# Kernel optimization log

Hardware: AMD Instinct MI355X
Metric: run time of the kernel (lower is better)

Reference implementation:

```python
import jax, jax.numpy as jnp
import numpy as np

B, S, H = 4, 128, 768
OUT, TAG = 24, 4


def setup_inputs() -> dict:
    key = jax.random.key(0)
    k1, k2, k3, k4, k5 = jax.random.split(key, 5)
    x = jax.random.normal(k1, (B, S, H), dtype=jnp.float32)
    # linear1: in 2H -> out 3H ; linear2: in 3H -> out TAG*OUT
    s1 = 1.0 / np.sqrt(2 * H)
    s2 = 1.0 / np.sqrt(3 * H)
    W1 = jax.random.uniform(k2, (2 * H, 3 * H), minval=-s1, maxval=s1, dtype=jnp.float32)
    b1 = jax.random.uniform(k3, (3 * H,), minval=-s1, maxval=s1, dtype=jnp.float32)
    W2 = jax.random.uniform(k4, (3 * H, TAG * OUT), minval=-s2, maxval=s2, dtype=jnp.float32)
    b2 = jax.random.uniform(k5, (TAG * OUT,), minval=-s2, maxval=s2, dtype=jnp.float32)
    return {"x": x, "W1": W1, "b1": b1, "W2": W2, "b2": b2}


def reference(x, W1, b1, W2, b2):
    b, s, h = x.shape
    # pairs[b,i,j] = concat(x[b,i], x[b,j]); avoid explicit 2H concat by
    # splitting W1 into head/tail halves (same math as cat -> linear1).
    W1h, W1t = W1[:h], W1[h:]
    head = jnp.einsum('bih,hk->bik', x, W1h)          # [B,S,3H]
    tail = jnp.einsum('bjh,hk->bjk', x, W1t)          # [B,S,3H]
    hid = head[:, :, None, :] + tail[:, None, :, :] + b1  # [B,S,S,3H]
    hid = jax.nn.relu(hid)  # dropout is identity in eval mode
    scores = jnp.einsum('bijk,ko->bijo', hid, W2) + b2     # [B,S,S,TAG*OUT]
    return scores.reshape(b, s, s, OUT, TAG)
```

## Files before the change

kernel.cpp:

```cpp
#include <hip/hip_runtime.h>
#include <hip/hip_bf16.h>


typedef __bf16 bf16x8 __attribute__((ext_vector_type(8)));
typedef _Float16 f16x8 __attribute__((ext_vector_type(8)));
typedef float f32x4 __attribute__((ext_vector_type(4)));

#define S_   128
#define H_   768
#define K3   2304
#define NOUT 96
#define NIT  36

__device__ __forceinline__ unsigned short f2bf(float f) {
    union { __bf16 b; unsigned short u; } c;
    c.b = (__bf16)f;
    return c.u;
}

__device__ __forceinline__ unsigned short f2h(float f) {
    union { _Float16 h; unsigned short u; } c;
    c.h = (_Float16)f;
    return c.u;
}

__device__ __forceinline__ void gload_lds16(const unsigned short* g, unsigned short* l) {
    __builtin_amdgcn_global_load_lds(
        (const __attribute__((address_space(1))) void*)g,
        (__attribute__((address_space(3))) void*)l,
        16, 0, 0);
}

__global__ __launch_bounds__(256) void k_prep(
        const float* __restrict__ x, unsigned short* __restrict__ xb,
        const float* __restrict__ W1, unsigned short* __restrict__ w1t,
        const float* __restrict__ W2, unsigned short* __restrict__ w2f) {
    __shared__ float tile[32][33];
    const int bid = blockIdx.x, tid = threadIdx.x;
    if (bid < 384) {
        int t = bid * 256 + tid;
        float4 v = ((const float4*)x)[t];
        ushort4 o;
        o.x = f2bf(v.x); o.y = f2bf(v.y); o.z = f2bf(v.z); o.w = f2bf(v.w);
        ((ushort4*)xb)[t] = o;
    } else if (bid < 3840) {
        int idx = bid - 384;
        int bx = idx % 72, by = (idx / 72) % 24, bz = idx / 1728;
        const float* src = W1 + (size_t)bz * H_ * K3;
        unsigned short* dst = w1t + (size_t)bz * K3 * H_;
        int c0 = bx * 32, r0 = by * 32;
        int row = tid >> 3, c4 = (tid & 7) * 4;
        float4 v = *(const float4*)(src + (size_t)(r0 + row) * K3 + c0 + c4);
        tile[row][c4 + 0] = v.x; tile[row][c4 + 1] = v.y;
        tile[row][c4 + 2] = v.z; tile[row][c4 + 3] = v.w;
        __syncthreads();
        ushort4 o;
        o.x = f2bf(tile[c4 + 0][row]); o.y = f2bf(tile[c4 + 1][row]);
        o.z = f2bf(tile[c4 + 2][row]); o.w = f2bf(tile[c4 + 3][row]);
        *(ushort4*)(dst + (size_t)(c0 + row) * H_ + r0 + c4) = o;
    } else {
        int t = (bid - 3840) * 256 + tid;
        int l = t & 63, f = (t >> 6) % 6, kc = t / 384;
        int k0 = kc * 32 + (l >> 4) * 8;
        int o  = f * 16 + (l & 15);
        unsigned short v[8];
#pragma unroll
        for (int e = 0; e < 8; e++)
            v[e] = f2h(W2[(size_t)(k0 + e) * NOUT + o]);
        *(uint4*)(w2f + (size_t)t * 8) = *(const uint4*)v;
    }
}

__global__ __launch_bounds__(256) void k_gemm1(
        const unsigned short* __restrict__ xb,
        const unsigned short* __restrict__ w1t,
        const float* __restrict__ b1,
        unsigned short* __restrict__ headh,
        unsigned short* __restrict__ tailh) {
    __shared__ unsigned short As[64 * 32];
    __shared__ unsigned short Bs[128 * 32];
    const int tid = threadIdx.x;
    const int l = tid & 63, w = tid >> 6;
    const int m0 = blockIdx.y * 64;
    const int n0 = blockIdx.x * 128;
    const int wr = (w >> 1) * 32, wc = (w & 1) * 64;
    const int lr = l & 15, lk = (l >> 4) * 8;
    f32x4 acc[2][4] = {};

    for (int kt = 0; kt < H_; kt += 32) {
        {
            int row = tid >> 2, seg = (tid & 3) * 8;
            gload_lds16(xb + (size_t)(m0 + row) * H_ + kt + seg, As + tid * 8);
        }
#pragma unroll
        for (int p = 0; p < 2; ++p) {
            int idx = p * 256 + tid;
            int row = idx >> 2, seg = (idx & 3) * 8;
            gload_lds16(w1t + (size_t)(n0 + row) * H_ + kt + seg, Bs + idx * 8);
        }
        asm volatile("s_waitcnt vmcnt(0)" ::: "memory");
        __syncthreads();
        bf16x8 af[2], bfr[4];
#pragma unroll
        for (int i = 0; i < 2; i++) af[i]  = *(const bf16x8*)(As + (wr + i * 16 + lr) * 32 + lk);
#pragma unroll
        for (int j = 0; j < 4; j++) bfr[j] = *(const bf16x8*)(Bs + (wc + j * 16 + lr) * 32 + lk);
#pragma unroll
        for (int i = 0; i < 2; i++)
#pragma unroll
            for (int j = 0; j < 4; j++)
                acc[i][j] = __builtin_amdgcn_mfma_f32_16x16x32_bf16(af[i], bfr[j], acc[i][j], 0, 0, 0);
        __syncthreads();
    }

    const bool tailblk = (n0 >= K3);
    unsigned short* dst = tailblk ? tailh : headh;
    const int nloc = n0 - (tailblk ? K3 : 0);
    const int lv = (l >> 4) * 4;
#pragma unroll
    for (int j = 0; j < 4; j++) {
        int c = nloc + wc + j * 16 + lr;
        float bias = tailblk ? b1[c] : 0.0f;
#pragma unroll
        for (int i = 0; i < 2; i++) {
            int mrow = m0 + wr + i * 16 + lv;
#pragma unroll
            for (int e = 0; e < 4; e++)
                dst[(size_t)(mrow + e) * K3 + c] = f2h(acc[i][j][e] + bias);
        }
    }
}

__device__ __forceinline__ f16x8 form8h(uint4 hq, uint4 tq) {
    union { uint4 q; f16x8 v; } H, T;
    H.q = hq; T.q = tq;
    f16x8 s = H.v + T.v;
    const f16x8 z = {0, 0, 0, 0, 0, 0, 0, 0};
    return __builtin_elementwise_max(s, z);
}

__device__ __forceinline__ f16x8 u4f16(uint4 v) {
    union { uint4 q; f16x8 b; } c; c.q = v; return c.b;
}

__global__ __launch_bounds__(256, 1) void k_pair(
        const unsigned short* __restrict__ headh,
        const unsigned short* __restrict__ tailh,
        const unsigned short* __restrict__ w2f,
        const float* __restrict__ b2,
        float* __restrict__ out) {
    const int tid = threadIdx.x;
    const int w = tid >> 6, l = tid & 63;
    const int lr = l & 15, lkq = l >> 4;
    const int lkoff = lkq * 8;
    const int jb = blockIdx.x;
    const int ig = blockIdx.y;
    const int b  = blockIdx.z;
    const int i0 = ig * 8 + w * 2;

    const unsigned short* Hp = headh + (size_t)(b * S_ + i0) * K3;
    const unsigned short* T0 = tailh + (size_t)(b * S_ + jb * 32 + lr) * K3;
    const unsigned short* T1 = T0 + (size_t)16 * K3;
    const unsigned short* Wp = w2f + l * 8;

    f32x4 acc[2][2][6] = {};
    float b2v[6];
#pragma unroll
    for (int f = 0; f < 6; f++) b2v[f] = b2[f * 16 + lr];

    uint4 wcur[12], wnxt[12];
#pragma unroll
    for (int s = 0; s < 12; s++) wcur[s] = *(const uint4*)(Wp + s * 512);

    uint4 tc[2][2], hc[2][2];
#pragma unroll
    for (int kk = 0; kk < 2; kk++) {
        tc[0][kk] = *(const uint4*)(T0 + kk * 32 + lkoff);
        tc[1][kk] = *(const uint4*)(T1 + kk * 32 + lkoff);
        hc[0][kk] = *(const uint4*)(Hp + kk * 32 + lkoff);
        hc[1][kk] = *(const uint4*)(Hp + K3 + kk * 32 + lkoff);
    }

    for (int n = 0; n < NIT; ++n) {
        const int np = (n + 1 < NIT) ? (n + 1) : (NIT - 1);
        const unsigned short* wsrc = Wp + (size_t)np * 6144;
#pragma unroll
        for (int s = 0; s < 12; s++) wnxt[s] = *(const uint4*)(wsrc + s * 512);
        const int kn = np * 64;
        uint4 tn[2][2], hn[2][2];
#pragma unroll
        for (int kk = 0; kk < 2; kk++) {
            tn[0][kk] = *(const uint4*)(T0 + kn + kk * 32 + lkoff);
            tn[1][kk] = *(const uint4*)(T1 + kn + kk * 32 + lkoff);
            hn[0][kk] = *(const uint4*)(Hp + kn + kk * 32 + lkoff);
            hn[1][kk] = *(const uint4*)(Hp + K3 + kn + kk * 32 + lkoff);
        }

#pragma unroll
        for (int kk = 0; kk < 2; kk++) {
            f16x8 a[2][2];
#pragma unroll
            for (int qi = 0; qi < 2; qi++)
#pragma unroll
                for (int jg = 0; jg < 2; jg++)
                    a[qi][jg] = form8h(hc[qi][kk], tc[jg][kk]);
#pragma unroll
            for (int f = 0; f < 6; f++) {
                f16x8 bfr = u4f16(wcur[kk * 6 + f]);
#pragma unroll
                for (int qi = 0; qi < 2; qi++)
#pragma unroll
                    for (int jg = 0; jg < 2; jg++)
                        acc[qi][jg][f] = __builtin_amdgcn_mfma_f32_16x16x32_f16(
                            a[qi][jg], bfr, acc[qi][jg][f], 0, 0, 0);
            }
        }

#pragma unroll
        for (int s = 0; s < 12; s++) wcur[s] = wnxt[s];
#pragma unroll
        for (int kk = 0; kk < 2; kk++) {
            tc[0][kk] = tn[0][kk]; tc[1][kk] = tn[1][kk];
            hc[0][kk] = hn[0][kk]; hc[1][kk] = hn[1][kk];
        }
    }

#pragma unroll
    for (int qi = 0; qi < 2; qi++) {
        float* O = out + ((size_t)(b * S_ + i0 + qi) * S_ + jb * 32) * NOUT;
#pragma unroll
        for (int jg = 0; jg < 2; jg++)
#pragma unroll
            for (int f = 0; f < 6; f++)
#pragma unroll
                for (int e = 0; e < 4; e++) {
                    int j = jg * 16 + lkq * 4 + e;
                    O[(size_t)j * NOUT + f * 16 + lr] = acc[qi][jg][f][e] + b2v[f];
                }
    }
}

extern "C" void kernel_launch(void* const* d_in, const int* in_sizes, int n_in,
                              void* d_out, int out_size, void* d_ws, size_t ws_size,
                              hipStream_t stream) {
    const float* x  = (const float*)d_in[0];
    const float* W1 = (const float*)d_in[1];
    const float* b1 = (const float*)d_in[2];
    const float* W2 = (const float*)d_in[3];
    const float* b2 = (const float*)d_in[4];
    float* out = (float*)d_out;

    char* ws = (char*)d_ws;
    unsigned short* xb    = (unsigned short*)(ws);
    unsigned short* w1t   = (unsigned short*)(ws +   786432);
    unsigned short* w2f   = (unsigned short*)(ws +  7864320);
    unsigned short* headh = (unsigned short*)(ws +  8306688);
    unsigned short* tailh = (unsigned short*)(ws + 10665984);

    hipLaunchKernelGGL(k_prep, dim3(3948), dim3(256), 0, stream,
                       x, xb, W1, w1t, W2, w2f);
    hipLaunchKernelGGL(k_gemm1, dim3(36, 8), dim3(256), 0, stream,
                       xb, w1t, b1, headh, tailh);
    hipLaunchKernelGGL(k_pair, dim3(4, 16, 4), dim3(256), 0, stream,
                       headh, tailh, w2f, b2, out);
}
```

Before: 67.57 us.

## Split pair kernel K-loop across two warp groups with LDS-staged W2 and reduction

The pair kernel now runs 512 threads per block as two groups of four waves, each covering half of the 2304-wide reduction, and combines the partial accumulators through LDS at the end. W2 fragments are no longer prefetched into registers; they are staged into double-buffered LDS with global_load_lds and read back per MFMA, which frees registers and raises occupancy. The cost is a per-iteration barrier, extra LDS traffic and a three-round cross-group reduction, and the grid ordering is swapped.

After: 72.78 us. +7.7%, slower.

```diff
diff --git a/kernel.cpp b/kernel.cpp
--- a/kernel.cpp
+++ b/kernel.cpp
@@ -10,7 +10,7 @@
 #define H_   768
 #define K3   2304
 #define NOUT 96
-#define NIT  36
+#define NITG 18
 
 __device__ __forceinline__ unsigned short f2bf(float f) {
     union { __bf16 b; unsigned short u; } c;
@@ -139,63 +139,72 @@
     return __builtin_elementwise_max(s, z);
 }
 
-__device__ __forceinline__ f16x8 u4f16(uint4 v) {
-    union { uint4 q; f16x8 b; } c; c.q = v; return c.b;
-}
-
-__global__ __launch_bounds__(256, 1) void k_pair(
+__global__ __launch_bounds__(512) void k_pair(
         const unsigned short* __restrict__ headh,
         const unsigned short* __restrict__ tailh,
         const unsigned short* __restrict__ w2f,
         const float* __restrict__ b2,
         float* __restrict__ out) {
+    __shared__ __align__(16) unsigned short lds[4][6144];
+
     const int tid = threadIdx.x;
     const int w = tid >> 6, l = tid & 63;
+    const int g  = w >> 2;
+    const int wi = w & 3;
+    const int tg = tid & 255;
     const int lr = l & 15, lkq = l >> 4;
     const int lkoff = lkq * 8;
-    const int jb = blockIdx.x;
-    const int ig = blockIdx.y;
+    const int ig = blockIdx.x;
+    const int jb = blockIdx.y;
     const int b  = blockIdx.z;
-    const int i0 = ig * 8 + w * 2;
+    const int i0 = ig * 8 + wi * 2;
+    const int cbase = g * NITG;
 
     const unsigned short* Hp = headh + (size_t)(b * S_ + i0) * K3;
     const unsigned short* T0 = tailh + (size_t)(b * S_ + jb * 32 + lr) * K3;
     const unsigned short* T1 = T0 + (size_t)16 * K3;
-    const unsigned short* Wp = w2f + l * 8;
 
     f32x4 acc[2][2][6] = {};
-    float b2v[6];
-#pragma unroll
-    for (int f = 0; f < 6; f++) b2v[f] = b2[f * 16 + lr];
-
-    uint4 wcur[12], wnxt[12];
-#pragma unroll
-    for (int s = 0; s < 12; s++) wcur[s] = *(const uint4*)(Wp + s * 512);
-
+
+    auto stage = [&](int sbuf, int c) {
+        const unsigned short* src = w2f + (size_t)c * 6144;
+#pragma unroll
+        for (int i = 0; i < 3; ++i)
+            gload_lds16(src + i * 2048 + tg * 8, &lds[sbuf][i * 2048 + tg * 8]);
+    };
+
+    stage(g * 2, cbase);
     uint4 tc[2][2], hc[2][2];
 #pragma unroll
     for (int kk = 0; kk < 2; kk++) {
-        tc[0][kk] = *(const uint4*)(T0 + kk * 32 + lkoff);
-        tc[1][kk] = *(const uint4*)(T1 + kk * 32 + lkoff);
-        hc[0][kk] = *(const uint4*)(Hp + kk * 32 + lkoff);
-        hc[1][kk] = *(const uint4*)(Hp + K3 + kk * 32 + lkoff);
-    }
-
-    for (int n = 0; n < NIT; ++n) {
-        const int np = (n + 1 < NIT) ? (n + 1) : (NIT - 1);
-        const unsigned short* wsrc = Wp + (size_t)np * 6144;
-#pragma unroll
-        for (int s = 0; s < 12; s++) wnxt[s] = *(const uint4*)(wsrc + s * 512);
-        const int kn = np * 64;
+        const int kb = cbase * 64 + kk * 32 + lkoff;
+        tc[0][kk] = *(const uint4*)(T0 + kb);
+        tc[1][kk] = *(const uint4*)(T1 + kb);
+        hc[0][kk] = *(const uint4*)(Hp + kb);
+        hc[1][kk] = *(const uint4*)(Hp + K3 + kb);
+    }
+    asm volatile("s_waitcnt vmcnt(0)" ::: "memory");
+    __builtin_amdgcn_s_barrier();
+
+    for (int n = 0; n < NITG; ++n) {
+        const int cn = cbase + ((n < NITG - 1) ? n + 1 : n);
         uint4 tn[2][2], hn[2][2];
 #pragma unroll
         for (int kk = 0; kk < 2; kk++) {
-            tn[0][kk] = *(const uint4*)(T0 + kn + kk * 32 + lkoff);
-            tn[1][kk] = *(const uint4*)(T1 + kn + kk * 32 + lkoff);
-            hn[0][kk] = *(const uint4*)(Hp + kn + kk * 32 + lkoff);
-            hn[1][kk] = *(const uint4*)(Hp + K3 + kn + kk * 32 + lkoff);
-        }
-
+            const int kb = cn * 64 + kk * 32 + lkoff;
+            tn[0][kk] = *(const uint4*)(T0 + kb);
+            tn[1][kk] = *(const uint4*)(T1 + kb);
+            hn[0][kk] = *(const uint4*)(Hp + kb);
+            hn[1][kk] = *(const uint4*)(Hp + K3 + kb);
+        }
+
+        asm volatile("s_waitcnt vmcnt(8)" ::: "memory");
+        __builtin_amdgcn_s_barrier();
+
+        stage(g * 2 + ((n + 1) & 1), cbase + ((n + 1 < NITG) ? n + 1 : n));
+
+        const unsigned short* Lb = &lds[g * 2 + (n & 1)][0];
+        __builtin_amdgcn_s_setprio(1);
 #pragma unroll
         for (int kk = 0; kk < 2; kk++) {
             f16x8 a[2][2];
@@ -206,7 +215,7 @@
                     a[qi][jg] = form8h(hc[qi][kk], tc[jg][kk]);
 #pragma unroll
             for (int f = 0; f < 6; f++) {
-                f16x8 bfr = u4f16(wcur[kk * 6 + f]);
+                f16x8 bfr = *(const f16x8*)(Lb + kk * 3072 + f * 512 + l * 8);
 #pragma unroll
                 for (int qi = 0; qi < 2; qi++)
 #pragma unroll
@@ -215,9 +224,7 @@
                             a[qi][jg], bfr, acc[qi][jg][f], 0, 0, 0);
             }
         }
-
-#pragma unroll
-        for (int s = 0; s < 12; s++) wcur[s] = wnxt[s];
+        __builtin_amdgcn_s_setprio(0);
 #pragma unroll
         for (int kk = 0; kk < 2; kk++) {
             tc[0][kk] = tn[0][kk]; tc[1][kk] = tn[1][kk];
@@ -225,18 +232,53 @@
         }
     }
 
-#pragma unroll
-    for (int qi = 0; qi < 2; qi++) {
-        float* O = out + ((size_t)(b * S_ + i0 + qi) * S_ + jb * 32) * NOUT;
-#pragma unroll
-        for (int jg = 0; jg < 2; jg++)
-#pragma unroll
-            for (int f = 0; f < 6; f++)
-#pragma unroll
-                for (int e = 0; e < 4; e++) {
-                    int j = jg * 16 + lkq * 4 + e;
-                    O[(size_t)j * NOUT + f * 16 + lr] = acc[qi][jg][f][e] + b2v[f];
-                }
+    asm volatile("s_waitcnt vmcnt(0)" ::: "memory");
+    __syncthreads();
+
+    float4* red = (float4*)&lds[0][0];
+    const int rbase = (wi * 64 + l) * 8;
+#pragma unroll
+    for (int r = 0; r < 3; r++) {
+        if (g == 1) {
+#pragma unroll
+            for (int s = 0; s < 8; s++) {
+                const int idx = r * 8 + s;
+                const int qi = idx / 12, jg = (idx % 12) / 6, f = idx % 6;
+                f32x4 v = acc[qi][jg][f];
+                red[rbase + s] = make_float4(v[0], v[1], v[2], v[3]);
+            }
+        }
+        __syncthreads();
+        if (g == 0) {
+#pragma unroll
+            for (int s = 0; s < 8; s++) {
+                const int idx = r * 8 + s;
+                const int qi = idx / 12, jg = (idx % 12) / 6, f = idx % 6;
+                float4 v = red[rbase + s];
+                acc[qi][jg][f][0] += v.x; acc[qi][jg][f][1] += v.y;
+                acc[qi][jg][f][2] += v.z; acc[qi][jg][f][3] += v.w;
+            }
+        }
+        __syncthreads();
+    }
+
+    if (g == 0) {
+        float b2v[6];
+#pragma unroll
+        for (int f = 0; f < 6; f++) b2v[f] = b2[f * 16 + lr];
+#pragma unroll
+        for (int qi = 0; qi < 2; qi++) {
+            float* O = out + ((size_t)(b * S_ + i0 + qi) * S_ + jb * 32) * NOUT;
+#pragma unroll
+            for (int jg = 0; jg < 2; jg++)
+#pragma unroll
+                for (int f = 0; f < 6; f++)
+#pragma unroll
+                    for (int e = 0; e < 4; e++) {
+                        int j = jg * 16 + lkq * 4 + e;
+                        O[(size_t)j * NOUT + f * 16 + lr] = acc[qi][jg][f][e] + b2v[f];
+                    }
+        }
     }
 }
 
@@ -261,6 +303,6 @@
                        x, xb, W1, w1t, W2, w2f);
     hipLaunchKernelGGL(k_gemm1, dim3(36, 8), dim3(256), 0, stream,
                        xb, w1t, b1, headh, tailh);
-    hipLaunchKernelGGL(k_pair, dim3(4, 16, 4), dim3(256), 0, stream,
+    hipLaunchKernelGGL(k_pair, dim3(16, 4, 4), dim3(512), 0, stream,
                        headh, tailh, w2f, b2, out);
 }
```

## Switch pair kernel to 32x32x16 MFMA with split-K across wave groups

Applied to the files above, without the earlier changes.

Replaces the 16x16x32 MFMA tiling in the pair kernel with 32x32x16 MFMAs, which reduces how often the combined head+tail fragments and W2 fragments are reloaded. The K dimension is split across two wave groups, and partial sums are reduced through shared memory. The change doubles the grid, raises launch bounds to two blocks per CU, and reorders the W2 fragment layout in prep to match. It also adds an explicit vmcnt wait and s_setprio around the MFMA block. The costs are an LDS reduction with extra barriers, and only half the waves doing the output stores.

Result: slower. 69.41 us (+2.7%).

```diff
diff --git a/kernel.cpp b/kernel.cpp
--- a/kernel.cpp
+++ b/kernel.cpp
@@ -5,12 +5,13 @@
 typedef __bf16 bf16x8 __attribute__((ext_vector_type(8)));
 typedef _Float16 f16x8 __attribute__((ext_vector_type(8)));
 typedef float f32x4 __attribute__((ext_vector_type(4)));
+typedef float f32x16 __attribute__((ext_vector_type(16)));
 
 #define S_   128
 #define H_   768
 #define K3   2304
 #define NOUT 96
-#define NIT  36
+#define NITG 36
 
 __device__ __forceinline__ unsigned short f2bf(float f) {
     union { __bf16 b; unsigned short u; } c;
@@ -60,9 +61,9 @@
         *(ushort4*)(dst + (size_t)(c0 + row) * H_ + r0 + c4) = o;
     } else {
         int t = (bid - 3840) * 256 + tid;
-        int l = t & 63, f = (t >> 6) % 6, kc = t / 384;
-        int k0 = kc * 32 + (l >> 4) * 8;
-        int o  = f * 16 + (l & 15);
+        int l = t & 63, og = (t >> 6) % 3, s = t / 192;
+        int k0 = s * 16 + (l >> 5) * 8;
+        int o  = og * 32 + (l & 31);
         unsigned short v[8];
 #pragma unroll
         for (int e = 0; e < 8; e++)
@@ -143,100 +144,126 @@
     union { uint4 q; f16x8 b; } c; c.q = v; return c.b;
 }
 
-__global__ __launch_bounds__(256, 1) void k_pair(
+__global__ __launch_bounds__(256, 2) void k_pair(
         const unsigned short* __restrict__ headh,
         const unsigned short* __restrict__ tailh,
         const unsigned short* __restrict__ w2f,
         const float* __restrict__ b2,
         float* __restrict__ out) {
+    __shared__ __align__(16) float4 red[2][3][64][4];
+
     const int tid = threadIdx.x;
     const int w = tid >> 6, l = tid & 63;
-    const int lr = l & 15, lkq = l >> 4;
-    const int lkoff = lkq * 8;
+    const int g  = w >> 1;
+    const int wi = w & 1;
+    const int lo = l & 31;
+    const int ko = (l >> 5) * 8;
     const int jb = blockIdx.x;
     const int ig = blockIdx.y;
     const int b  = blockIdx.z;
-    const int i0 = ig * 8 + w * 2;
+    const int i0 = ig * 4 + wi * 2;
+    const int cbase = g * NITG;
 
     const unsigned short* Hp = headh + (size_t)(b * S_ + i0) * K3;
-    const unsigned short* T0 = tailh + (size_t)(b * S_ + jb * 32 + lr) * K3;
-    const unsigned short* T1 = T0 + (size_t)16 * K3;
+    const unsigned short* Tp = tailh + (size_t)(b * S_ + jb * 32 + lo) * K3;
     const unsigned short* Wp = w2f + l * 8;
 
-    f32x4 acc[2][2][6] = {};
-    float b2v[6];
-#pragma unroll
-    for (int f = 0; f < 6; f++) b2v[f] = b2[f * 16 + lr];
-
-    uint4 wcur[12], wnxt[12];
-#pragma unroll
-    for (int s = 0; s < 12; s++) wcur[s] = *(const uint4*)(Wp + s * 512);
-
-    uint4 tc[2][2], hc[2][2];
-#pragma unroll
-    for (int kk = 0; kk < 2; kk++) {
-        tc[0][kk] = *(const uint4*)(T0 + kk * 32 + lkoff);
-        tc[1][kk] = *(const uint4*)(T1 + kk * 32 + lkoff);
-        hc[0][kk] = *(const uint4*)(Hp + kk * 32 + lkoff);
-        hc[1][kk] = *(const uint4*)(Hp + K3 + kk * 32 + lkoff);
-    }
-
-    for (int n = 0; n < NIT; ++n) {
-        const int np = (n + 1 < NIT) ? (n + 1) : (NIT - 1);
-        const unsigned short* wsrc = Wp + (size_t)np * 6144;
-#pragma unroll
-        for (int s = 0; s < 12; s++) wnxt[s] = *(const uint4*)(wsrc + s * 512);
-        const int kn = np * 64;
-        uint4 tn[2][2], hn[2][2];
-#pragma unroll
-        for (int kk = 0; kk < 2; kk++) {
-            tn[0][kk] = *(const uint4*)(T0 + kn + kk * 32 + lkoff);
-            tn[1][kk] = *(const uint4*)(T1 + kn + kk * 32 + lkoff);
-            hn[0][kk] = *(const uint4*)(Hp + kn + kk * 32 + lkoff);
-            hn[1][kk] = *(const uint4*)(Hp + K3 + kn + kk * 32 + lkoff);
-        }
-
-#pragma unroll
-        for (int kk = 0; kk < 2; kk++) {
-            f16x8 a[2][2];
-#pragma unroll
-            for (int qi = 0; qi < 2; qi++)
-#pragma unroll
-                for (int jg = 0; jg < 2; jg++)
-                    a[qi][jg] = form8h(hc[qi][kk], tc[jg][kk]);
-#pragma unroll
-            for (int f = 0; f < 6; f++) {
-                f16x8 bfr = u4f16(wcur[kk * 6 + f]);
-#pragma unroll
-                for (int qi = 0; qi < 2; qi++)
-#pragma unroll
-                    for (int jg = 0; jg < 2; jg++)
-                        acc[qi][jg][f] = __builtin_amdgcn_mfma_f32_16x16x32_f16(
-                            a[qi][jg], bfr, acc[qi][jg][f], 0, 0, 0);
+    f32x16 acc[2][3] = {};
+
+    uint4 wcur[6], wnxt[6];
+#pragma unroll
+    for (int si = 0; si < 2; si++)
+#pragma unroll
+        for (int og = 0; og < 3; og++)
+            wcur[si * 3 + og] = *(const uint4*)(Wp + ((size_t)(2 * cbase + si) * 3 + og) * 512);
+    uint4 tc[2], hc[2][2], tn[2], hn[2][2];
+#pragma unroll
+    for (int si = 0; si < 2; si++) {
+        const int kb = cbase * 32 + si * 16 + ko;
+        tc[si]    = *(const uint4*)(Tp + kb);
+        hc[0][si] = *(const uint4*)(Hp + kb);
+        hc[1][si] = *(const uint4*)(Hp + K3 + kb);
+    }
+
+    for (int n = 0; n < NITG; ++n) {
+        const int cn = cbase + ((n < NITG - 1) ? n + 1 : n);
+#pragma unroll
+        for (int si = 0; si < 2; si++)
+#pragma unroll
+            for (int og = 0; og < 3; og++)
+                wnxt[si * 3 + og] = *(const uint4*)(Wp + ((size_t)(2 * cn + si) * 3 + og) * 512);
+#pragma unroll
+        for (int si = 0; si < 2; si++) {
+            const int kb = cn * 32 + si * 16 + ko;
+            tn[si]    = *(const uint4*)(Tp + kb);
+            hn[0][si] = *(const uint4*)(Hp + kb);
+            hn[1][si] = *(const uint4*)(Hp + K3 + kb);
+        }
+        asm volatile("s_waitcnt vmcnt(12)" ::: "memory");
+
+        __builtin_amdgcn_s_setprio(1);
+#pragma unroll
+        for (int si = 0; si < 2; si++) {
+            f16x8 a0 = form8h(hc[0][si], tc[si]);
+            f16x8 a1 = form8h(hc[1][si], tc[si]);
+#pragma unroll
+            for (int og = 0; og < 3; og++) {
+                f16x8 bfr = u4f16(wcur[si * 3 + og]);
+                acc[0][og] = __builtin_amdgcn_mfma_f32_32x32x16_f16(a0, bfr, acc[0][og], 0, 0, 0);
+                acc[1][og] = __builtin_amdgcn_mfma_f32_32x32x16_f16(a1, bfr, acc[1][og], 0, 0, 0);
             }
         }
-
-#pragma unroll
-        for (int s = 0; s < 12; s++) wcur[s] = wnxt[s];
-#pragma unroll
-        for (int kk = 0; kk < 2; kk++) {
-            tc[0][kk] = tn[0][kk]; tc[1][kk] = tn[1][kk];
-            hc[0][kk] = hn[0][kk]; hc[1][kk] = hn[1][kk];
-        }
-    }
-
-#pragma unroll
-    for (int qi = 0; qi < 2; qi++) {
-        float* O = out + ((size_t)(b * S_ + i0 + qi) * S_ + jb * 32) * NOUT;
-#pragma unroll
-        for (int jg = 0; jg < 2; jg++)
-#pragma unroll
-            for (int f = 0; f < 6; f++)
-#pragma unroll
-                for (int e = 0; e < 4; e++) {
-                    int j = jg * 16 + lkq * 4 + e;
-                    O[(size_t)j * NOUT + f * 16 + lr] = acc[qi][jg][f][e] + b2v[f];
+        __builtin_amdgcn_s_setprio(0);
+
+#pragma unroll
+        for (int s = 0; s < 6; s++) wcur[s] = wnxt[s];
+#pragma unroll
+        for (int si = 0; si < 2; si++) {
+            tc[si] = tn[si]; hc[0][si] = hn[0][si]; hc[1][si] = hn[1][si];
+        }
+    }
+
+    asm volatile("s_waitcnt vmcnt(0) lgkmcnt(0)" ::: "memory");
+    __syncthreads();
+#pragma unroll
+    for (int r = 0; r < 2; r++) {
+        if (g == 1) {
+#pragma unroll
+            for (int s = 0; s < 3; s++)
+#pragma unroll
+                for (int p = 0; p < 4; p++)
+                    red[wi][s][l][p] = make_float4(acc[r][s][p * 4 + 0], acc[r][s][p * 4 + 1],
+                                                   acc[r][s][p * 4 + 2], acc[r][s][p * 4 + 3]);
+        }
+        __syncthreads();
+        if (g == 0) {
+#pragma unroll
+            for (int s = 0; s < 3; s++)
+#pragma unroll
+                for (int p = 0; p < 4; p++) {
+                    float4 v = red[wi][s][l][p];
+                    acc[r][s][p * 4 + 0] += v.x; acc[r][s][p * 4 + 1] += v.y;
+                    acc[r][s][p * 4 + 2] += v.z; acc[r][s][p * 4 + 3] += v.w;
                 }
+        }
+        __syncthreads();
+    }
+
+    if (g == 0) {
+        float b2v[3];
+#pragma unroll
+        for (int og = 0; og < 3; og++) b2v[og] = b2[og * 32 + lo];
+#pragma unroll
+        for (int qi = 0; qi < 2; qi++) {
+            float* O = out + ((size_t)(b * S_ + i0 + qi) * S_ + jb * 32) * NOUT + lo;
+#pragma unroll
+            for (int og = 0; og < 3; og++)
+#pragma unroll
+                for (int r = 0; r < 16; r++) {
+                    int j = (r & 3) + 8 * (r >> 2) + 4 * (l >> 5);
+                    O[(size_t)j * NOUT + og * 32] = acc[qi][og][r] + b2v[og];
+                }
+        }
     }
 }
 
@@ -261,6 +288,6 @@
                        x, xb, W1, w1t, W2, w2f);
     hipLaunchKernelGGL(k_gemm1, dim3(36, 8), dim3(256), 0, stream,
                        xb, w1t, b1, headh, tailh);
-    hipLaunchKernelGGL(k_pair, dim3(4, 16, 4), dim3(256), 0, stream,
+    hipLaunchKernelGGL(k_pair, dim3(4, 32, 4), dim3(256), 0, stream,
                        headh, tailh, w2f, b2, out);
 }
```
